# Performance work log

Measured on AMD Instinct MI355X. Metric: run time of the kernel, lower is better.

The kernel has to match this reference:

```python
import jax, jax.numpy as jnp
import numpy as np

N_NODES = 50000
N_EDGES = 800000
IN_DIM = 64
OUT_DIM = 64
LEAKY_SLOPE = 0.01  # torch default negative_slope


def setup_inputs() -> dict:
    key = jax.random.key(0)
    k1, k2, k3, k4 = jax.random.split(key, 4)
    x = jax.random.normal(k1, (N_NODES, IN_DIM), dtype=jnp.float32)
    edge_index = jax.random.randint(k2, (2, N_EDGES), 0, N_NODES, dtype=jnp.int64)
    # Linear weights, torch-style [out, in], scaled like kaiming-uniform-ish init
    W1 = jax.random.normal(k3, (OUT_DIM, 2 * IN_DIM), dtype=jnp.float32) / np.sqrt(2 * IN_DIM)
    b1 = jnp.zeros((OUT_DIM,), dtype=jnp.float32)
    W2 = jax.random.normal(k4, (OUT_DIM, OUT_DIM), dtype=jnp.float32) / np.sqrt(OUT_DIM)
    b2 = jnp.zeros((OUT_DIM,), dtype=jnp.float32)
    return {"x": x, "edge_index": edge_index, "W1": W1, "b1": b1, "W2": W2, "b2": b2}


def reference(x, edge_index, W1, b1, W2, b2):
    # PyG convention: edge_index[0] = source j, edge_index[1] = target i
    src, dst = edge_index[0], edge_index[1]
    x_i = x[dst]                     # [E, D] target features
    x_j = x[src]                     # [E, D] source features
    tmp = jnp.concatenate([x_i, x_j - x_i], axis=1)  # [E, 2D]
    h = tmp @ W1.T + b1              # [E, out]
    h = jnp.where(h >= 0, h, LEAKY_SLOPE * h)        # LeakyReLU
    msg = h @ W2.T + b2              # [E, out]
    # scatter-max aggregate to targets; empty segments -> 0 (PyG fill)
    agg = jax.ops.segment_max(msg, dst, num_segments=x.shape[0])
    agg = jnp.where(jnp.isfinite(agg), agg, 0.0)
    return jnp.tanh(agg)
```

## Files before the change

kernel.cpp:

```cpp
#include <hip/hip_runtime.h>
#include <hip/hip_bf16.h>
#include <math.h>

#define N_NODES 50000
#define N_EDGES 800000
#define CAP 32
#define MAX_OVF 8192

#define NBIN 196
#define KA_BLOCKS 256
#define EPB (N_EDGES / KA_BLOCKS)
#define SUBCAP 48

#define UV_BLOCKS 256
#define W2_BLOCKS 16
#define P1_GRID (KA_BLOCKS + UV_BLOCKS + W2_BLOCKS)

typedef _Float16 f16x8 __attribute__((ext_vector_type(8)));
typedef float f32x4 __attribute__((ext_vector_type(4)));

__global__ __launch_bounds__(256) void phase1_kernel(
    const float* __restrict__ x, const float* __restrict__ W1,
    const float* __restrict__ b1, const float* __restrict__ W2,
    const int* __restrict__ ei,
    _Float16* __restrict__ Uh, _Float16* __restrict__ Vh,
    _Float16* __restrict__ w2f,
    unsigned* __restrict__ arena, unsigned* __restrict__ cntA,
    unsigned* __restrict__ cur, int2* __restrict__ ovf)
{
    __shared__ unsigned sh_hist[256];
    __shared__ unsigned sh_pack[EPB];
    __shared__ unsigned short sh_rank[EPB];

    const int blk = blockIdx.x;
    const int tid = threadIdx.x;

    if (blk < KA_BLOCKS) {
        sh_hist[tid] = 0;
        __syncthreads();
        const int e0 = blk * EPB;
        for (int i = tid; i < EPB; i += 256) {
            int s = ei[e0 + i];
            int d = ei[N_EDGES + e0 + i];
            unsigned bin = (unsigned)d >> 8;
            unsigned r = atomicAdd(&sh_hist[bin], 1u);
            sh_pack[i] = (unsigned)s | ((unsigned)(d & 255) << 16) | (bin << 24);
            sh_rank[i] = (unsigned short)r;
        }
        __syncthreads();
        if (tid < NBIN) cntA[tid * KA_BLOCKS + blk] = sh_hist[tid];
        const unsigned base = cur[0];
        for (int i = tid; i < EPB; i += 256) {
            unsigned p = sh_pack[i];
            unsigned r = sh_rank[i];
            unsigned bin = p >> 24;
            if (r < SUBCAP) {
                arena[((size_t)bin * KA_BLOCKS + blk) * SUBCAP + r] = p;
            } else {
                atomicAdd(&cur[32], 1u);
                unsigned o = atomicAdd(&cur[16], 1u) - base;
                int d = (int)(bin * 256 + ((p >> 16) & 255u));
                int s = (int)(p & 0xFFFFu);
                if (o < MAX_OVF) ovf[o] = make_int2(d, s);
            }
        }
    } else if (blk < KA_BLOCKS + UV_BLOCKS) {
        const int lane = tid & 63;
        const int m = lane & 15;
        const int q = lane >> 4;
        const int wv  = ((blk - KA_BLOCKS) * 256 + tid) >> 6;
        const int nwv = UV_BLOCKS * 4;

        f16x8 wafr[4][2], wbfr[4][2];
#pragma unroll
        for (int t = 0; t < 4; ++t) {
            const float* w1r = W1 + (size_t)(t * 16 + m) * 128;
#pragma unroll
            for (int s = 0; s < 2; ++s) {
                const int c0 = 32 * s + q * 8;
                float4 pa0 = *(const float4*)(w1r + c0);
                float4 pa1 = *(const float4*)(w1r + c0 + 4);
                float4 pb0 = *(const float4*)(w1r + 64 + c0);
                float4 pb1 = *(const float4*)(w1r + 64 + c0 + 4);
                float av[8] = {pa0.x, pa0.y, pa0.z, pa0.w,
                               pa1.x, pa1.y, pa1.z, pa1.w};
                float bv[8] = {pb0.x, pb0.y, pb0.z, pb0.w,
                               pb1.x, pb1.y, pb1.z, pb1.w};
#pragma unroll
                for (int j = 0; j < 8; ++j) {
                    wafr[t][s][j] = (_Float16)(av[j] - bv[j]);
                    wbfr[t][s][j] = (_Float16)bv[j];
                }
            }
        }
        float biasv[4];
#pragma unroll
        for (int t = 0; t < 4; ++t) biasv[t] = b1[t * 16 + m];

        for (int tile = wv; tile < N_NODES / 16; tile += nwv) {
            const float* xr = x + (size_t)(tile * 16 + m) * 64 + q * 8;
            f16x8 a[2];
#pragma unroll
            for (int s = 0; s < 2; ++s) {
                float4 x0 = *(const float4*)(xr + 32 * s);
                float4 x1 = *(const float4*)(xr + 32 * s + 4);
                float xv[8] = {x0.x, x0.y, x0.z, x0.w, x1.x, x1.y, x1.z, x1.w};
#pragma unroll
                for (int j = 0; j < 8; ++j) a[s][j] = (_Float16)xv[j];
            }
#pragma unroll
            for (int t = 0; t < 4; ++t) {
                f32x4 au = {0.f, 0.f, 0.f, 0.f};
                f32x4 aw = {0.f, 0.f, 0.f, 0.f};
                au = __builtin_amdgcn_mfma_f32_16x16x32_f16(a[0], wafr[t][0], au, 0, 0, 0);
                au = __builtin_amdgcn_mfma_f32_16x16x32_f16(a[1], wafr[t][1], au, 0, 0, 0);
                aw = __builtin_amdgcn_mfma_f32_16x16x32_f16(a[0], wbfr[t][0], aw, 0, 0, 0);
                aw = __builtin_amdgcn_mfma_f32_16x16x32_f16(a[1], wbfr[t][1], aw, 0, 0, 0);
#pragma unroll
                for (int r = 0; r < 4; ++r) {
                    const size_t row = (size_t)(tile * 16 + 4 * q + r) * 64;
                    Uh[row + t * 16 + m] = (_Float16)(au[r] + biasv[t]);
                    Vh[row + t * 16 + m] = (_Float16)aw[r];
                }
            }
        }
    } else {
        const int i = (blk - KA_BLOCKS - UV_BLOCKS) * 256 + tid;
        if (i < 64 * 64) w2f[i] = (_Float16)W2[i];
    }
}

__global__ __launch_bounds__(1024) void bucket_kernel(
    const unsigned* __restrict__ arena, const unsigned* __restrict__ cntA,
    unsigned* __restrict__ counts, unsigned short* __restrict__ buckets,
    unsigned* __restrict__ cur, int2* __restrict__ ovf)
{
    __shared__ unsigned lcnt[256];
    const int bin = blockIdx.x;
    const int tid = threadIdx.x;
    if (tid < 256) lcnt[tid] = 0;
    __syncthreads();

    const unsigned base = cur[0];
    const int chunk = tid & 255;
    const int part  = tid >> 8;
    unsigned n = cntA[(size_t)bin * KA_BLOCKS + chunk];
    if (n > SUBCAP) n = SUBCAP;
    const unsigned j0 = (n * (unsigned)part) >> 2;
    const unsigned j1 = (n * (unsigned)(part + 1)) >> 2;
    const unsigned* ch = arena + ((size_t)bin * KA_BLOCKS + chunk) * SUBCAP;

    for (unsigned j = j0; j < j1; ++j) {
        unsigned p = ch[j];
        unsigned dlow = (p >> 16) & 255u;
        unsigned s = p & 0xFFFFu;
        unsigned pos = atomicAdd(&lcnt[dlow], 1u);
        int d = bin * 256 + (int)dlow;
        if (pos < CAP) {
            buckets[(size_t)d * CAP + pos] = (unsigned short)s;
        } else {
            unsigned o = atomicAdd(&cur[16], 1u) - base;
            if (o < MAX_OVF) ovf[o] = make_int2(d, (int)s);
        }
    }
    __syncthreads();
    if (tid < 256) {
        const int node = bin * 256 + tid;
        if (node < N_NODES) counts[node] = lcnt[tid];
    }
}

__device__ __forceinline__ void tile_mfma_max(
    const f16x8* __restrict__ uh, const f16x8* __restrict__ vv,
    const _Float16* __restrict__ w2f, int m, int q, int lim,
    float* __restrict__ rm)
{
    f16x8 a[2];
#pragma unroll
    for (int s = 0; s < 2; ++s) {
        f16x8 h  = uh[s] + vv[s];
        f16x8 hs = h * (_Float16)0.01f;
#pragma unroll
        for (int j = 0; j < 8; ++j)
            a[s][j] = (h[j] > hs[j]) ? h[j] : hs[j];
    }
#pragma unroll
    for (int t = 0; t < 4; ++t) {
        const f16x8 b0 = *(const f16x8*)(w2f + (t * 16 + m) * 64 + q * 8);
        const f16x8 b1 = *(const f16x8*)(w2f + (t * 16 + m) * 64 + 32 + q * 8);
        f32x4 acc = {0.f, 0.f, 0.f, 0.f};
        acc = __builtin_amdgcn_mfma_f32_16x16x32_f16(a[0], b0, acc, 0, 0, 0);
        acc = __builtin_amdgcn_mfma_f32_16x16x32_f16(a[1], b1, acc, 0, 0, 0);
        float v = -INFINITY;
#pragma unroll
        for (int r = 0; r < 4; ++r)
            if (4 * q + r < lim) v = fmaxf(v, acc[r]);
        rm[t] = fmaxf(rm[t], v);
    }
}

__device__ __forceinline__ void load_vh(const _Float16* __restrict__ Vh,
                                        unsigned si, int q, f16x8* vv)
{
    const _Float16* b0 = Vh + (size_t)si * 64 + q * 8;
    vv[0] = *(const f16x8*)b0;
    vv[1] = *(const f16x8*)(b0 + 32);
}

__device__ __forceinline__ float fast_tanh(float x)
{
    float xc = fminf(fmaxf(x, -12.f), 12.f);
    float e  = __expf(2.f * xc);
    return 1.f - 2.f * __builtin_amdgcn_rcpf(e + 1.f);
}

__global__ __launch_bounds__(256, 4) void node_kernel(
    const unsigned* __restrict__ counts, const unsigned short* __restrict__ buckets,
    const int2* __restrict__ ovf,
    const _Float16* __restrict__ Uh, const _Float16* __restrict__ Vh,
    const _Float16* __restrict__ w2f, const float* __restrict__ b2,
    float* __restrict__ out, const unsigned* __restrict__ cur)
{
    const int lane = threadIdx.x & 63;
    const int m    = lane & 15;
    const int q    = lane >> 4;
    const int wave = (int)((blockIdx.x * blockDim.x + threadIdx.x) >> 6);
    const int nwav = (int)((gridDim.x * blockDim.x) >> 6);

    const float b2v = b2[lane];
    const unsigned base  = cur[0];
    const unsigned force = cur[32] - base;
    const unsigned nou   = cur[16] - base;

    const int nA0 = wave;
    int pB = nA0 + nwav; if (pB >= N_NODES) pB = N_NODES - 1;

    unsigned cntA = counts[nA0];
    int bktA  = buckets[nA0 * CAP + m];
    int bkt2A = buckets[nA0 * CAP + 16 + m];
    f16x8 uhA[2];
    load_vh(Uh, (unsigned)nA0, q, uhA);
    unsigned cntB = counts[pB];
    int bktB  = buckets[pB * CAP + m];
    int bkt2B = buckets[pB * CAP + 16 + m];

    f16x8 vA[2];
    {
        unsigned usiA = (unsigned)bktA;
        if (usiA >= N_NODES) usiA = N_NODES - 1;
        load_vh(Vh, usiA, q, vA);
    }
    f16x8 uhB[2];
    load_vh(Uh, (unsigned)pB, q, uhB);

    for (int n = nA0; n < N_NODES; n += nwav) {
        int pC = n + 2 * nwav; if (pC >= N_NODES) pC = N_NODES - 1;

        unsigned usiB = (unsigned)bktB;
        if (usiB >= N_NODES) usiB = N_NODES - 1;
        f16x8 vB[2];
        load_vh(Vh, usiB, q, vB);

        unsigned cntC = counts[pC];
        int bktC  = buckets[pC * CAP + m];
        int bkt2C = buckets[pC * CAP + 16 + m];

        const unsigned c = cntA;
        const int deg = (c < CAP) ? (int)c : CAP;

        float rm[4] = {-INFINITY, -INFINITY, -INFINITY, -INFINITY};
        const int lim0 = (deg < 16) ? deg : 16;
        tile_mfma_max(uhA, vA, w2f, m, q, lim0, rm);

        if (deg > 16) {
            unsigned si2 = (unsigned)bkt2A;
            if (si2 >= N_NODES) si2 = N_NODES - 1;
            f16x8 v2[2];
            load_vh(Vh, si2, q, v2);
            tile_mfma_max(uhA, v2, w2f, m, q, deg - 16, rm);
        }

        if (c > CAP || force != 0u) {
            int no = (nou < MAX_OVF) ? (int)nou : MAX_OVF;
            for (int o = 0; o < no; ++o) {
                const int2 ds = ovf[o];
                if (ds.x != n) continue;
                f16x8 vo[2];
                load_vh(Vh, (unsigned)ds.y, q, vo);
                tile_mfma_max(uhA, vo, w2f, m, q, 16, rm);
            }
        }

#pragma unroll
        for (int t = 0; t < 4; ++t) {
            rm[t] = fmaxf(rm[t], __shfl_xor(rm[t], 16, 64));
            rm[t] = fmaxf(rm[t], __shfl_xor(rm[t], 32, 64));
        }
        const float sel = (q == 0) ? rm[0] : (q == 1) ? rm[1]
                        : (q == 2) ? rm[2] : rm[3];
        out[(size_t)n * 64 + lane] = (c != 0u) ? fast_tanh(sel + b2v) : 0.f;

        cntA = cntB; cntB = cntC;
        bktB = bktC; bkt2A = bkt2B; bkt2B = bkt2C;
#pragma unroll
        for (int i = 0; i < 2; ++i) { uhA[i] = uhB[i]; vA[i] = vB[i]; }
        load_vh(Uh, (unsigned)pC, q, uhB);
    }
}

extern "C" void kernel_launch(void* const* d_in, const int* in_sizes, int n_in,
                              void* d_out, int out_size, void* d_ws, size_t ws_size,
                              hipStream_t stream)
{
    const float* x  = (const float*)d_in[0];
    const int*   ei = (const int*)d_in[1];
    const float* W1 = (const float*)d_in[2];
    const float* b1 = (const float*)d_in[3];
    const float* W2 = (const float*)d_in[4];
    const float* b2 = (const float*)d_in[5];
    float* out = (float*)d_out;

    char* p = (char*)d_ws;
    _Float16* Uh = (_Float16*)p;           p += (size_t)N_NODES * 64 * 2;
    _Float16* Vh = (_Float16*)p;           p += (size_t)N_NODES * 64 * 2;
    unsigned* arena = (unsigned*)p;        p += (size_t)NBIN * KA_BLOCKS * SUBCAP * 4;
    unsigned short* buckets = (unsigned short*)p;
                                           p += (size_t)N_NODES * CAP * 2;
    _Float16* w2f = (_Float16*)p;          p += 64 * 64 * 2;
    unsigned* cntA = (unsigned*)p;         p += (size_t)NBIN * KA_BLOCKS * 4;
    unsigned* counts = (unsigned*)p;       p += (size_t)((N_NODES + 63) / 64) * 64 * 4;
    unsigned* cur = (unsigned*)p;          p += 64 * 4;
    int2* ovf = (int2*)p;                  p += (size_t)MAX_OVF * 8;

    phase1_kernel<<<P1_GRID, 256, 0, stream>>>(x, W1, b1, W2, ei,
                                               Uh, Vh, w2f,
                                               arena, cntA, cur, ovf);
    bucket_kernel<<<NBIN, 1024, 0, stream>>>(arena, cntA, counts, buckets, cur, ovf);
    node_kernel<<<1024, 256, 0, stream>>>(counts, buckets, ovf,
                                          Uh, Vh, w2f, b2, out, cur);
}
```

Baseline: 130.8 us.

## Locally counting-sort edges per block into compact arena, drop fixed-capacity subchunks

Each partition block now builds a histogram, does an exclusive scan in shared memory, and scatters its edges into a bin-sorted shared buffer. The buffer is written contiguously to global memory with vector stores, and per-block offsets are recorded. This replaces the padded per-bin SUBCAP subchunks and their global-atomic overflow path, which cuts arena footprint and scattered writes. The cost is an extra pass over the destination indices and a serial scan with many barriers.

After: 133.6 us. 2.2% more time.

```diff
diff --git a/kernel.cpp b/kernel.cpp
--- a/kernel.cpp
+++ b/kernel.cpp
@@ -10,7 +10,7 @@
 #define NBIN 196
 #define KA_BLOCKS 256
 #define EPB (N_EDGES / KA_BLOCKS)
-#define SUBCAP 48
+#define EPB4 3128
 
 #define UV_BLOCKS 256
 #define W2_BLOCKS 16
@@ -26,44 +26,54 @@
     _Float16* __restrict__ Uh, _Float16* __restrict__ Vh,
     _Float16* __restrict__ w2f,
     unsigned* __restrict__ arena, unsigned* __restrict__ cntA,
-    unsigned* __restrict__ cur, int2* __restrict__ ovf)
+    unsigned* __restrict__ offs)
 {
     __shared__ unsigned sh_hist[256];
-    __shared__ unsigned sh_pack[EPB];
-    __shared__ unsigned short sh_rank[EPB];
+    __shared__ unsigned sh_scan[256];
+    __shared__ unsigned sh_cur[256];
+    __shared__ unsigned sh_sorted[EPB4];
 
     const int blk = blockIdx.x;
     const int tid = threadIdx.x;
 
     if (blk < KA_BLOCKS) {
         sh_hist[tid] = 0;
+        if (tid < EPB4 - EPB) sh_sorted[EPB + tid] = 0;
         __syncthreads();
         const int e0 = blk * EPB;
+        for (int i = tid; i < EPB; i += 256)
+            atomicAdd(&sh_hist[(unsigned)ei[N_EDGES + e0 + i] >> 8], 1u);
+        __syncthreads();
+
+        unsigned v = sh_hist[tid];
+        sh_scan[tid] = v;
+        __syncthreads();
+        for (int off = 1; off < 256; off <<= 1) {
+            unsigned t = (tid >= off) ? sh_scan[tid - off] : 0u;
+            __syncthreads();
+            sh_scan[tid] += t;
+            __syncthreads();
+        }
+        const unsigned excl = sh_scan[tid] - v;
+        sh_cur[tid] = excl;
+        if (tid < NBIN) {
+            cntA[(size_t)blk * NBIN + tid] = v;
+            offs[(size_t)blk * NBIN + tid] = excl;
+        }
+        __syncthreads();
+
         for (int i = tid; i < EPB; i += 256) {
             int s = ei[e0 + i];
             int d = ei[N_EDGES + e0 + i];
             unsigned bin = (unsigned)d >> 8;
-            unsigned r = atomicAdd(&sh_hist[bin], 1u);
-            sh_pack[i] = (unsigned)s | ((unsigned)(d & 255) << 16) | (bin << 24);
-            sh_rank[i] = (unsigned short)r;
-        }
-        __syncthreads();
-        if (tid < NBIN) cntA[tid * KA_BLOCKS + blk] = sh_hist[tid];
-        const unsigned base = cur[0];
-        for (int i = tid; i < EPB; i += 256) {
-            unsigned p = sh_pack[i];
-            unsigned r = sh_rank[i];
-            unsigned bin = p >> 24;
-            if (r < SUBCAP) {
-                arena[((size_t)bin * KA_BLOCKS + blk) * SUBCAP + r] = p;
-            } else {
-                atomicAdd(&cur[32], 1u);
-                unsigned o = atomicAdd(&cur[16], 1u) - base;
-                int d = (int)(bin * 256 + ((p >> 16) & 255u));
-                int s = (int)(p & 0xFFFFu);
-                if (o < MAX_OVF) ovf[o] = make_int2(d, s);
-            }
-        }
+            unsigned dst = atomicAdd(&sh_cur[bin], 1u);
+            sh_sorted[dst] = (unsigned)s | ((unsigned)(d & 255) << 16) | (bin << 24);
+        }
+        __syncthreads();
+
+        uint4* dst4 = (uint4*)(arena + (size_t)blk * EPB4);
+        const uint4* src4 = (const uint4*)sh_sorted;
+        for (int i = tid; i < EPB4 / 4; i += 256) dst4[i] = src4[i];
     } else if (blk < KA_BLOCKS + UV_BLOCKS) {
         const int lane = tid & 63;
         const int m = lane & 15;
@@ -132,6 +142,7 @@
 
 __global__ __launch_bounds__(1024) void bucket_kernel(
     const unsigned* __restrict__ arena, const unsigned* __restrict__ cntA,
+    const unsigned* __restrict__ offs,
     unsigned* __restrict__ counts, unsigned short* __restrict__ buckets,
     unsigned* __restrict__ cur, int2* __restrict__ ovf)
 {
@@ -144,11 +155,11 @@
     const unsigned base = cur[0];
     const int chunk = tid & 255;
     const int part  = tid >> 8;
-    unsigned n = cntA[(size_t)bin * KA_BLOCKS + chunk];
-    if (n > SUBCAP) n = SUBCAP;
+    const unsigned n  = cntA[(size_t)chunk * NBIN + bin];
+    const unsigned st = offs[(size_t)chunk * NBIN + bin];
     const unsigned j0 = (n * (unsigned)part) >> 2;
     const unsigned j1 = (n * (unsigned)(part + 1)) >> 2;
-    const unsigned* ch = arena + ((size_t)bin * KA_BLOCKS + chunk) * SUBCAP;
+    const unsigned* ch = arena + (size_t)chunk * EPB4 + st;
 
     for (unsigned j = j0; j < j1; ++j) {
         unsigned p = ch[j];
@@ -235,7 +246,7 @@
     const int nA0 = wave;
     int pB = nA0 + nwav; if (pB >= N_NODES) pB = N_NODES - 1;
 
-    unsigned cntA = counts[nA0];
+    unsigned cntAa = counts[nA0];
     int bktA  = buckets[nA0 * CAP + m];
     int bkt2A = buckets[nA0 * CAP + 16 + m];
     f16x8 uhA[2];
@@ -265,7 +276,7 @@
         int bktC  = buckets[pC * CAP + m];
         int bkt2C = buckets[pC * CAP + 16 + m];
 
-        const unsigned c = cntA;
+        const unsigned c = cntAa;
         const int deg = (c < CAP) ? (int)c : CAP;
 
         float rm[4] = {-INFINITY, -INFINITY, -INFINITY, -INFINITY};
@@ -300,7 +311,7 @@
                         : (q == 2) ? rm[2] : rm[3];
         out[(size_t)n * 64 + lane] = (c != 0u) ? fast_tanh(sel + b2v) : 0.f;
 
-        cntA = cntB; cntB = cntC;
+        cntAa = cntB; cntB = cntC;
         bktB = bktC; bkt2A = bkt2B; bkt2B = bkt2C;
 #pragma unroll
         for (int i = 0; i < 2; ++i) { uhA[i] = uhB[i]; vA[i] = vB[i]; }
@@ -323,19 +334,21 @@
     char* p = (char*)d_ws;
     _Float16* Uh = (_Float16*)p;           p += (size_t)N_NODES * 64 * 2;
     _Float16* Vh = (_Float16*)p;           p += (size_t)N_NODES * 64 * 2;
-    unsigned* arena = (unsigned*)p;        p += (size_t)NBIN * KA_BLOCKS * SUBCAP * 4;
+    unsigned* arena = (unsigned*)p;        p += (size_t)KA_BLOCKS * EPB4 * 4;
     unsigned short* buckets = (unsigned short*)p;
                                            p += (size_t)N_NODES * CAP * 2;
     _Float16* w2f = (_Float16*)p;          p += 64 * 64 * 2;
-    unsigned* cntA = (unsigned*)p;         p += (size_t)NBIN * KA_BLOCKS * 4;
+    unsigned* cntA = (unsigned*)p;         p += (size_t)KA_BLOCKS * NBIN * 4;
+    unsigned* offs = (unsigned*)p;         p += (size_t)KA_BLOCKS * NBIN * 4;
     unsigned* counts = (unsigned*)p;       p += (size_t)((N_NODES + 63) / 64) * 64 * 4;
     unsigned* cur = (unsigned*)p;          p += 64 * 4;
     int2* ovf = (int2*)p;                  p += (size_t)MAX_OVF * 8;
 
     phase1_kernel<<<P1_GRID, 256, 0, stream>>>(x, W1, b1, W2, ei,
                                                Uh, Vh, w2f,
-                                               arena, cntA, cur, ovf);
-    bucket_kernel<<<NBIN, 1024, 0, stream>>>(arena, cntA, counts, buckets, cur, ovf);
+                                               arena, cntA, offs);
+    bucket_kernel<<<NBIN, 1024, 0, stream>>>(arena, cntA, offs,
+                                             counts, buckets, cur, ovf);
     node_kernel<<<1024, 256, 0, stream>>>(counts, buckets, ovf,
                                           Uh, Vh, w2f, b2, out, cur);
 }
```
